# Kernel tuning notes

Measured on AMD Instinct MI355X. Metric: run time of the kernel, lower is better.

The kernel has to match this reference:

```python
import jax, jax.numpy as jnp
import numpy as np

ALPHA = 0.2  # leaky_relu negative slope (init arg `alpha`)
V_NODES = 7

def setup_inputs() -> dict:
    key = jax.random.key(0)
    k1, k2, k3 = jax.random.split(key, 3)
    N, C, T, V = 256, 256, 64, V_NODES
    IN, OUT = C * T, 256
    h = jax.random.normal(k1, (N, C, T, V), dtype=jnp.float32)
    # xavier_uniform with gain=1.414
    limW = 1.414 * np.sqrt(6.0 / (IN + OUT))
    W = jax.random.uniform(k2, (IN, OUT), dtype=jnp.float32, minval=-limW, maxval=limW)
    lima = 1.414 * np.sqrt(6.0 / (2 * OUT + 1))
    a = jax.random.uniform(k3, (2 * OUT, 1), dtype=jnp.float32, minval=-lima, maxval=lima)
    Bp = jnp.zeros((V, V), dtype=jnp.float32)  # torch: zeros(7,7)+1e-6; the 1e-6 is added in reference
    return {"h": h, "W": W, "a": a, "Bp": Bp}

def reference(h, W, a, Bp):
    N, C, T, V = h.shape
    E = W.shape[1]
    # (N,C,T,V) -> (N,V,C*T)
    hf = jnp.transpose(h, (0, 3, 1, 2)).reshape(N, V, C * T)
    Wh = jnp.einsum('nvi,io->nvo', hf, W)  # [N,V,E]
    # pairwise concat score [Wh_i || Wh_j] @ a  ==  Wh_i@a1 + Wh_j@a2 (exact same math, no O(V^2*2E) tensor)
    a1, a2 = a[:E, 0], a[E:, 0]
    s1 = Wh @ a1  # [N,V] (score contribution of row node i)
    s2 = Wh @ a2  # [N,V] (score contribution of col node j)
    e = jax.nn.leaky_relu(s1[:, :, None] + s2[:, None, :], negative_slope=ALPHA)  # [N,V,V]
    attention = jax.nn.softmax(e, axis=-1)
    # learned adjacency: B + I, min-max normalized, sym-normalized D^-1/2 A D^-1/2
    adj = (Bp + 1e-6) + jnp.eye(V, dtype=Bp.dtype)
    adj = (adj - adj.min()) / (adj.max() - adj.min())
    D = jnp.diag(jnp.sum(adj, axis=1))
    D12 = jnp.sqrt(jnp.linalg.inv(D))  # diag -> elementwise sqrt of 1/deg on diagonal
    adj_norm = D12 @ adj @ D12  # [V,V]
    attention = jnp.einsum('ij,njk->nik', adj_norm, attention)  # [N,V,V]
    h_prime = jnp.einsum('nij,njo->nio', attention, Wh)  # [N,V,E]
    return jax.nn.elu(h_prime)
```

## Files before the change

kernel.cpp:

```cpp
#include <hip/hip_runtime.h>
#include <cstdint>

#define KK 16384
#define EE 256
#define M_USED 1792
#define LRELU_ALPHA 0.2f

typedef __bf16 bf16x8 __attribute__((ext_vector_type(8)));
typedef float f32x4 __attribute__((ext_vector_type(4)));

#define WT_BYTES (256u*16384u*2u)

__device__ __forceinline__ unsigned short f2bf(float f){
  union { float f; unsigned u; } x; x.f = f;
  unsigned r = x.u + 0x7fffu + ((x.u >> 16) & 1u);
  return (unsigned short)(r >> 16);
}

__global__ __launch_bounds__(256) void k_transpose_w(const float* __restrict__ W,
                                                     unsigned short* __restrict__ Wt){
  __shared__ float tile[64][65];
  const int i0 = blockIdx.x * 64;
  const int o0 = blockIdx.y * 64;
  const int tid = threadIdx.x;
  #pragma unroll
  for (int r = 0; r < 16; ++r){
    int il = r*4 + (tid >> 6);
    int ol = tid & 63;
    tile[il][ol] = W[(size_t)(i0+il)*EE + o0 + ol];
  }
  __syncthreads();
  #pragma unroll
  for (int r = 0; r < 16; ++r){
    int ol = r*4 + (tid >> 6);
    int il = tid & 63;
    Wt[(size_t)(o0+ol)*KK + i0 + il] = f2bf(tile[il][ol]);
  }
}

__global__ __launch_bounds__(512, 4) void k_gemm(const float* __restrict__ h,
                                                 const unsigned short* __restrict__ Wt,
                                                 _Float16* __restrict__ part,
                                                 int cpp ){
  __shared__ unsigned short Bs[2][64*136];
  const int tid  = threadIdx.x;
  const int nper = gridDim.x >> 3;
  const int id   = blockIdx.x;
  const int wid  = (id & 7)*nper + (id >> 3);
  const int mt   = wid & 31;
  const int kc   = wid >> 5;
  const int n0   = mt * 8;
  const int w    = tid >> 6;
  const int lane = tid & 63;
  const int col  = lane & 15;
  const int quad = lane >> 4;

  for (int idx = tid; idx < 1088; idx += 512){
    Bs[0][7616 + idx] = 0;
    Bs[1][7616 + idx] = 0;
  }

  int ghb[4]; short hlds[4][4];
  const bool hv3 = (tid < 256);
  #pragma unroll
  for (int it = 0; it < 4; ++it){
    int j  = tid + it*512;
    if (j >= 1792) j = 0;
    int p  = j / 896;
    int jj = j - p*896;
    int nn = jj / 112;
    int f  = jj - nn*112;
    ghb[it] = (n0+nn)*114688 + p*448 + f*4;
    #pragma unroll
    for (int e = 0; e < 4; ++e){
      int rr = f*4 + e;
      int t_ = rr / 7;
      int v_ = rr - t_*7;
      hlds[it][e] = (short)((nn*7 + v_)*136 + p*64 + t_);
    }
  }

  const unsigned short* aptr = Wt + (size_t)(w*32 + col)*KK + quad*8;

  f32x4 acc[2][4];
  #pragma unroll
  for (int a_ = 0; a_ < 2; ++a_)
    #pragma unroll
    for (int b_ = 0; b_ < 4; ++b_)
      acc[a_][b_] = (f32x4){0.f, 0.f, 0.f, 0.f};

  const int c0    = kc * cpp;
  const int iters = cpp >> 1;

  float4 hreg[4];
  {
    const int cb = c0*448;
    #pragma unroll
    for (int it = 0; it < 4; ++it)
      if (it < 3 || hv3)
        hreg[it] = *reinterpret_cast<const float4*>(h + (size_t)(ghb[it] + cb));
  }

  int buf = 0;
  for (int s = 0; s < iters; ++s){
    #pragma unroll
    for (int it = 0; it < 4; ++it){
      if (it < 3 || hv3){
        Bs[buf][hlds[it][0]] = f2bf(hreg[it].x);
        Bs[buf][hlds[it][1]] = f2bf(hreg[it].y);
        Bs[buf][hlds[it][2]] = f2bf(hreg[it].z);
        Bs[buf][hlds[it][3]] = f2bf(hreg[it].w);
      }
    }
    const int kb = (c0 + 2*s)*64;
    bf16x8 af[2][4];
    #pragma unroll
    for (int oi = 0; oi < 2; ++oi)
      #pragma unroll
      for (int kh = 0; kh < 4; ++kh)
        af[oi][kh] = *reinterpret_cast<const bf16x8*>(aptr + (size_t)oi*16*KK + kb + kh*32);
    if (s + 1 < iters){
      const int cb = (c0 + 2*(s+1))*448;
      #pragma unroll
      for (int it = 0; it < 4; ++it)
        if (it < 3 || hv3)
          hreg[it] = *reinterpret_cast<const float4*>(h + (size_t)(ghb[it] + cb));
    }
    __syncthreads();
    #pragma unroll
    for (int kh = 0; kh < 4; ++kh){
      bf16x8 bfr[4];
      #pragma unroll
      for (int mi = 0; mi < 4; ++mi)
        bfr[mi] = *reinterpret_cast<const bf16x8*>(&Bs[buf][(mi*16 + col)*136 + kh*32 + quad*8]);
      #pragma unroll
      for (int oi = 0; oi < 2; ++oi)
        #pragma unroll
        for (int mi = 0; mi < 4; ++mi)
          acc[oi][mi] = __builtin_amdgcn_mfma_f32_16x16x32_bf16(af[oi][kh], bfr[mi], acc[oi][mi], 0, 0, 0);
    }
    buf ^= 1;
  }

  #pragma unroll
  for (int oi = 0; oi < 2; ++oi){
    #pragma unroll
    for (int r = 0; r < 4; ++r){
      int o = w*32 + oi*16 + quad*4 + r;
      size_t rowbase = ((size_t)(kc*256 + o))*M_USED + mt*56;
      #pragma unroll
      for (int mi = 0; mi < 4; ++mi){
        int ml = mi*16 + col;
        if (ml < 56) part[rowbase + ml] = (_Float16)acc[oi][mi][r];
      }
    }
  }
}

__global__ __launch_bounds__(256) void k_reduce(const _Float16* __restrict__ part,
                                                float* __restrict__ Wh, int nkc){
  const int m = blockIdx.x*256 + threadIdx.x;
  const int o = blockIdx.y;
  float s = 0.f;
  for (int k = 0; k < nkc; ++k)
    s += (float)part[((size_t)(k*256 + o))*M_USED + m];
  Wh[(size_t)o*M_USED + m] = s;
}

__global__ __launch_bounds__(256) void k_attn(const float* __restrict__ Wh,
                                              const float* __restrict__ a,
                                              const float* __restrict__ Bp,
                                              float* __restrict__ out){
  const int n    = blockIdx.x;
  const int tid  = threadIdx.x;
  const int lane = tid & 63;
  const int wv   = tid >> 6;

  __shared__ float adjn[49];
  __shared__ float red1[4][7], red2[4][7];
  __shared__ float s1s[7], s2s[7];
  __shared__ float att0[49], att[49];

  if (tid == 0){
    float adj[49];
    float mn = 1e30f, mx = -1e30f;
    for (int i = 0; i < 7; ++i)
      for (int j = 0; j < 7; ++j){
        float x = Bp[i*7+j] + 1e-6f + (i == j ? 1.f : 0.f);
        adj[i*7+j] = x;
        mn = fminf(mn, x); mx = fmaxf(mx, x);
      }
    float inv = 1.f / (mx - mn);
    for (int i = 0; i < 49; ++i) adj[i] = (adj[i] - mn) * inv;
    float d12[7];
    for (int i = 0; i < 7; ++i){
      float s = 0.f;
      for (int j = 0; j < 7; ++j) s += adj[i*7+j];
      d12[i] = 1.f / sqrtf(s);
    }
    for (int i = 0; i < 7; ++i)
      for (int j = 0; j < 7; ++j)
        adjn[i*7+j] = d12[i] * adj[i*7+j] * d12[j];
  }

  float wh[7];
  #pragma unroll
  for (int v = 0; v < 7; ++v)
    wh[v] = Wh[(size_t)tid*M_USED + n*7 + v];

  const float a1 = a[tid];
  const float a2 = a[256 + tid];

  #pragma unroll
  for (int v = 0; v < 7; ++v){
    float x1 = wh[v]*a1;
    float x2 = wh[v]*a2;
    #pragma unroll
    for (int off = 32; off > 0; off >>= 1){
      x1 += __shfl_down(x1, off);
      x2 += __shfl_down(x2, off);
    }
    if (lane == 0){ red1[wv][v] = x1; red2[wv][v] = x2; }
  }
  __syncthreads();
  if (tid < 7){
    s1s[tid] = red1[0][tid]+red1[1][tid]+red1[2][tid]+red1[3][tid];
    s2s[tid] = red2[0][tid]+red2[1][tid]+red2[2][tid]+red2[3][tid];
  }
  __syncthreads();
  if (tid < 7){
    const int v = tid;
    float e[7]; float mx = -1e30f;
    #pragma unroll
    for (int u = 0; u < 7; ++u){
      float t = s1s[v] + s2s[u];
      t = t > 0.f ? t : LRELU_ALPHA*t;
      e[u] = t; mx = fmaxf(mx, t);
    }
    float sum = 0.f;
    #pragma unroll
    for (int u = 0; u < 7; ++u){ e[u] = expf(e[u]-mx); sum += e[u]; }
    float inv = 1.f/sum;
    #pragma unroll
    for (int u = 0; u < 7; ++u) att0[v*7+u] = e[u]*inv;
  }
  __syncthreads();
  if (tid < 7){
    const int v = tid;
    #pragma unroll
    for (int u = 0; u < 7; ++u){
      float s = 0.f;
      #pragma unroll
      for (int w7 = 0; w7 < 7; ++w7) s += adjn[v*7+w7]*att0[w7*7+u];
      att[v*7+u] = s;
    }
  }
  __syncthreads();
  #pragma unroll
  for (int v = 0; v < 7; ++v){
    float hp = 0.f;
    #pragma unroll
    for (int u = 0; u < 7; ++u) hp += att[v*7+u]*wh[u];
    float o = hp > 0.f ? hp : expm1f(hp);
    out[(size_t)(n*7+v)*256 + tid] = o;
  }
}

extern "C" void kernel_launch(void* const* d_in, const int* in_sizes, int n_in,
                              void* d_out, int out_size, void* d_ws, size_t ws_size,
                              hipStream_t stream){
  const float* h  = (const float*)d_in[0];
  const float* W  = (const float*)d_in[1];
  const float* a  = (const float*)d_in[2];
  const float* Bp = (const float*)d_in[3];
  float* out = (float*)d_out;
  char* ws = (char*)d_ws;

  const size_t part_elems = (size_t)256 * M_USED;
  const size_t need16 = WT_BYTES + 16 * part_elems * 2 + part_elems * 4;
  const int nkc = (ws_size >= need16) ? 16 : 8;

  unsigned short* Wt   = (unsigned short*)ws;
  _Float16*       part = (_Float16*)(ws + WT_BYTES);
  float*          Wh   = (float*)(ws + WT_BYTES + (size_t)nkc * part_elems * 2);

  k_transpose_w<<<dim3(256, 4), 256, 0, stream>>>(W, Wt);
  k_gemm<<<dim3(32 * nkc), 512, 0, stream>>>(h, Wt, part, 256/nkc);
  k_reduce<<<dim3(7, 256), 256, 0, stream>>>(part, Wh, nkc);
  k_attn<<<256, 256, 0, stream>>>(Wh, a, Bp, out);
}
```

Measured before the change: 213.3 us.

## Fuse split-K reduction into attention kernel and transpose partial layout

Removes the separate split-K reduce kernel and its intermediate Wh buffer. The attention kernel now sums the fp16 partials directly. The partials layout changes to be output-channel-contiguous, so the GEMM epilogue writes 4-wide vectorized fp16 stores and the attention kernel reads coalesced per-thread columns. This saves one kernel launch and one global round trip, at the cost of each attention block doing nkc strided reads.

Result: no change. 211.7 us (median of 2 runs) (-0.7%).

```diff
diff --git a/kernel.cpp b/kernel.cpp
--- a/kernel.cpp
+++ b/kernel.cpp
@@ -8,6 +8,7 @@
 
 typedef __bf16 bf16x8 __attribute__((ext_vector_type(8)));
 typedef float f32x4 __attribute__((ext_vector_type(4)));
+typedef _Float16 f16x4 __attribute__((ext_vector_type(4)));
 
 #define WT_BYTES (256u*16384u*2u)
 
@@ -144,33 +145,27 @@
 
   #pragma unroll
   for (int oi = 0; oi < 2; ++oi){
-    #pragma unroll
-    for (int r = 0; r < 4; ++r){
-      int o = w*32 + oi*16 + quad*4 + r;
-      size_t rowbase = ((size_t)(kc*256 + o))*M_USED + mt*56;
-      #pragma unroll
-      for (int mi = 0; mi < 4; ++mi){
-        int ml = mi*16 + col;
-        if (ml < 56) part[rowbase + ml] = (_Float16)acc[oi][mi][r];
+    const int ob = w*32 + oi*16 + quad*4;
+    #pragma unroll
+    for (int mi = 0; mi < 4; ++mi){
+      int ml = mi*16 + col;
+      if (ml < 56){
+        size_t idx = ((size_t)kc*M_USED + mt*56 + ml)*256 + ob;
+        f16x4 v;
+        v[0] = (_Float16)acc[oi][mi][0];
+        v[1] = (_Float16)acc[oi][mi][1];
+        v[2] = (_Float16)acc[oi][mi][2];
+        v[3] = (_Float16)acc[oi][mi][3];
+        *reinterpret_cast<f16x4*>(part + idx) = v;
       }
     }
   }
 }
 
-__global__ __launch_bounds__(256) void k_reduce(const _Float16* __restrict__ part,
-                                                float* __restrict__ Wh, int nkc){
-  const int m = blockIdx.x*256 + threadIdx.x;
-  const int o = blockIdx.y;
-  float s = 0.f;
-  for (int k = 0; k < nkc; ++k)
-    s += (float)part[((size_t)(k*256 + o))*M_USED + m];
-  Wh[(size_t)o*M_USED + m] = s;
-}
-
-__global__ __launch_bounds__(256) void k_attn(const float* __restrict__ Wh,
+__global__ __launch_bounds__(256) void k_attn(const _Float16* __restrict__ part,
                                               const float* __restrict__ a,
                                               const float* __restrict__ Bp,
-                                              float* __restrict__ out){
+                                              float* __restrict__ out, int nkc){
   const int n    = blockIdx.x;
   const int tid  = threadIdx.x;
   const int lane = tid & 63;
@@ -205,8 +200,13 @@
 
   float wh[7];
   #pragma unroll
-  for (int v = 0; v < 7; ++v)
-    wh[v] = Wh[(size_t)tid*M_USED + n*7 + v];
+  for (int v = 0; v < 7; ++v) wh[v] = 0.f;
+  for (int kc = 0; kc < nkc; ++kc){
+    const _Float16* p = part + ((size_t)kc*M_USED + n*7)*256 + tid;
+    #pragma unroll
+    for (int v = 0; v < 7; ++v)
+      wh[v] += (float)p[(size_t)v*256];
+  }
 
   const float a1 = a[tid];
   const float a2 = a[256 + tid];
@@ -277,15 +277,13 @@
   char* ws = (char*)d_ws;
 
   const size_t part_elems = (size_t)256 * M_USED;
-  const size_t need16 = WT_BYTES + 16 * part_elems * 2 + part_elems * 4;
+  const size_t need16 = WT_BYTES + 16 * part_elems * 2;
   const int nkc = (ws_size >= need16) ? 16 : 8;
 
   unsigned short* Wt   = (unsigned short*)ws;
   _Float16*       part = (_Float16*)(ws + WT_BYTES);
-  float*          Wh   = (float*)(ws + WT_BYTES + (size_t)nkc * part_elems * 2);
 
   k_transpose_w<<<dim3(256, 4), 256, 0, stream>>>(W, Wt);
   k_gemm<<<dim3(32 * nkc), 512, 0, stream>>>(h, Wt, part, 256/nkc);
-  k_reduce<<<dim3(7, 256), 256, 0, stream>>>(part, Wh, nkc);
-  k_attn<<<256, 256, 0, stream>>>(Wh, a, Bp, out);
-}
+  k_attn<<<256, 256, 0, stream>>>(part, a, Bp, out, nkc);
+}
```
